# Optimization experiments

Hardware: AMD Instinct MI355X
Metric: run time of the kernel (lower is better)

## Reference

```python
import jax, jax.numpy as jnp
import numpy as np

N = 8192
EPS = 1e-12

def setup_inputs() -> dict:
    key = jax.random.key(0)
    k1, k2 = jax.random.split(key)
    var_1 = jax.random.normal(k1, (N,), dtype=jnp.float32)          # e.g. bb mass
    var_2 = jax.random.uniform(k2, (N,), dtype=jnp.float32)          # classifier output in (0,1)
    normedweight = jnp.ones((N,), dtype=jnp.float32)                 # weights sum to N
    return {"var_1": var_1, "var_2": var_2, "normedweight": normedweight, "power": 2}


def reference(var_1, var_2, normedweight, power):
    # Pairwise absolute difference matrices [N, N]
    amat = jnp.abs(var_1[:, None] - var_1[None, :])
    bmat = jnp.abs(var_2[:, None] - var_2[None, :])

    # Weighted row means (weight broadcasts along columns, mean over axis=1)
    amatavg = jnp.mean(amat * normedweight, axis=1)                  # [N]
    bmatavg = jnp.mean(bmat * normedweight, axis=1)                  # [N]

    # Double centering: minuend_1[i,j] = avg[j], minuend_2[i,j] = avg[i]
    Amat = amat - amatavg[None, :] - amatavg[:, None] + jnp.mean(amatavg * normedweight)
    Bmat = bmat - bmatavg[None, :] - bmatavg[:, None] + jnp.mean(bmatavg * normedweight)

    ABavg = jnp.abs(jnp.mean(Amat * Bmat * normedweight, axis=1))    # [N]
    AAavg = jnp.mean(Amat * Amat * normedweight, axis=1)             # [N]
    BBavg = jnp.mean(Bmat * Bmat * normedweight, axis=1)             # [N]

    num = jnp.mean(ABavg * normedweight)
    den = jnp.abs(jnp.mean(AAavg * normedweight) * jnp.mean(BBavg * normedweight))

    if power == 1:
        dCorr = num / jnp.sqrt(den + EPS)
    elif power == 2:
        dCorr = num ** 2 / (den + EPS)
    else:
        dCorr = (num / jnp.sqrt(jnp.mean(AAavg * normedweight) * jnp.mean(BBavg * normedweight)) + EPS) ** power

    # Original clamps NaN and negative results to 0
    dCorr = jnp.where(jnp.isnan(dCorr), jnp.float32(0.0), dCorr)
    dCorr = jnp.maximum(dCorr, jnp.float32(0.0))
    return dCorr
```

## Files before the change

### kernel.cpp

```cpp
#include <hip/hip_runtime.h>
#include <math.h>


#define NN 8192
#define BLK 256
#define RPT 4
#define ROWS_PER_BLOCK 16
#define GRIDX 512
#define CSPLIT 4
#define SEGC 2048
#define ITERS 8
#define NBLK (GRIDX * CSPLIT)
#define MIDB 32
#define RPT2 8
#define G2BLK (NN / RPT2)
#define INV_N (1.0f / NN)
#define NSC 9

__device__ __forceinline__ void p1_elem(
    float aj, float bj, float wj,
    const float* __restrict__ ai, const float* __restrict__ bi,
    float* __restrict__ sa, float* __restrict__ sb) {
#pragma unroll
  for (int m = 0; m < RPT; ++m) {
    sa[m] = fmaf(fabsf(ai[m] - aj), wj, sa[m]);
    sb[m] = fmaf(fabsf(bi[m] - bj), wj, sb[m]);
  }
}

__global__ __launch_bounds__(BLK) void k_pass1(
    const float* __restrict__ a, const float* __restrict__ b,
    const float* __restrict__ w,
    float* __restrict__ pa, float* __restrict__ pb,
    double* __restrict__ gpa, double* __restrict__ gpb) {
  const int lane = threadIdx.x & 63;
  const int wv = threadIdx.x >> 6;
  const int i0 = blockIdx.x * ROWS_PER_BLOCK + wv * RPT;
  const int seg = blockIdx.y;

  float ai[RPT], bi[RPT], sa[RPT], sb[RPT];
#pragma unroll
  for (int m = 0; m < RPT; ++m) {
    ai[m] = a[i0 + m]; bi[m] = b[i0 + m];
    sa[m] = 0.f; sb[m] = 0.f;
  }

  const int jb = seg * SEGC;
  const float4* a4 = (const float4*)(a + jb) + lane;
  const float4* b4 = (const float4*)(b + jb) + lane;
  const float4* w4 = (const float4*)(w + jb) + lane;

  float4 A0 = a4[0], B0 = b4[0], W0 = w4[0];
#pragma unroll 1
  for (int k = 0; k < ITERS - 1; ++k) {
    const int nx = (k + 1) * 64;
    const float4 A1 = a4[nx], B1 = b4[nx], W1 = w4[nx];
    p1_elem(A0.x, B0.x, W0.x, ai, bi, sa, sb);
    p1_elem(A0.y, B0.y, W0.y, ai, bi, sa, sb);
    p1_elem(A0.z, B0.z, W0.z, ai, bi, sa, sb);
    p1_elem(A0.w, B0.w, W0.w, ai, bi, sa, sb);
    A0 = A1; B0 = B1; W0 = W1;
  }
  p1_elem(A0.x, B0.x, W0.x, ai, bi, sa, sb);
  p1_elem(A0.y, B0.y, W0.y, ai, bi, sa, sb);
  p1_elem(A0.z, B0.z, W0.z, ai, bi, sa, sb);
  p1_elem(A0.w, B0.w, W0.w, ai, bi, sa, sb);

#pragma unroll
  for (int off = 32; off >= 1; off >>= 1) {
#pragma unroll
    for (int m = 0; m < RPT; ++m) {
      sa[m] += __shfl_xor(sa[m], off);
      sb[m] += __shfl_xor(sb[m], off);
    }
  }

  __shared__ double gla[4], glb[4];
  if (lane == 0) {
#pragma unroll
    for (int m = 0; m < RPT; ++m) {
      pa[seg * NN + i0 + m] = sa[m];
      pb[seg * NN + i0 + m] = sb[m];
    }
    double da = 0.0, db = 0.0;
#pragma unroll
    for (int m = 0; m < RPT; ++m) {
      const double wi = (double)w[i0 + m];
      da += (double)sa[m] * wi;
      db += (double)sb[m] * wi;
    }
    gla[wv] = da; glb[wv] = db;
  }
  __syncthreads();
  if (threadIdx.x == 0) {
    const int bid = blockIdx.y * GRIDX + blockIdx.x;
    gpa[bid] = gla[0] + gla[1] + gla[2] + gla[3];
    gpb[bid] = glb[0] + glb[1] + glb[2] + glb[3];
  }
}

__global__ __launch_bounds__(BLK) void k_mid(
    const float* __restrict__ a, const float* __restrict__ b,
    const float* __restrict__ w,
    const float* __restrict__ pa, const float* __restrict__ pb,
    const double* __restrict__ gpa, const double* __restrict__ gpb,
    float* __restrict__ rr, float* __restrict__ ss, float* __restrict__ wrv,
    double* __restrict__ scal, double* __restrict__ hs) {
  const int lane = threadIdx.x & 63;
  const int wv = threadIdx.x >> 6;

  __shared__ double gsum[2];
  if (wv < 2) {
    const double* g = wv ? gpb : gpa;
    double s = 0.0;
    for (int k = 0; k < NBLK / 64; ++k) s += g[lane + 64 * k];
#pragma unroll
    for (int off = 32; off >= 1; off >>= 1) s += __shfl_xor(s, off);
    if (lane == 0) gsum[wv] = s;
  }
  __syncthreads();
  const double n2 = (double)NN * (double)NN;
  const float ha = (float)(0.5 * gsum[0] / n2);
  const float hb = (float)(0.5 * gsum[1] / n2);
  if (blockIdx.x == 0 && threadIdx.x == 0) { hs[0] = (double)ha; hs[1] = (double)hb; }

  const int i = blockIdx.x * BLK + threadIdx.x;
  const float av = (pa[i] + pa[NN + i] + pa[2 * NN + i] + pa[3 * NN + i]) * INV_N;
  const float bv = (pb[i] + pb[NN + i] + pb[2 * NN + i] + pb[3 * NN + i]) * INV_N;
  const float ri = av - ha;
  const float si = bv - hb;
  const float wi = w[i], aiv = a[i], biv = b[i];
  rr[i] = ri;  ss[i] = si;  wrv[i] = wi * ri;

  double p[NSC];
  p[0] = (double)wi;
  p[1] = (double)wi * aiv;
  p[2] = (double)wi * aiv * aiv;
  p[3] = (double)wi * biv;
  p[4] = (double)wi * biv * biv;
  p[5] = (double)wi * ri;
  p[6] = (double)wi * si;
  p[7] = (double)wi * ri * ri;
  p[8] = (double)wi * si * si;
#pragma unroll
  for (int off = 32; off >= 1; off >>= 1) {
#pragma unroll
    for (int t = 0; t < NSC; ++t) p[t] += __shfl_xor(p[t], off);
  }
  __shared__ double lp[NSC][4];
  if (lane == 0) {
#pragma unroll
    for (int t = 0; t < NSC; ++t) lp[t][wv] = p[t];
  }
  __syncthreads();
  if (threadIdx.x == 0) {
#pragma unroll
    for (int t = 0; t < NSC; ++t)
      scal[t * MIDB + blockIdx.x] = lp[t][0] + lp[t][1] + lp[t][2] + lp[t][3];
  }
}

__global__ __launch_bounds__(BLK) void k_pass2(
    const float* __restrict__ a, const float* __restrict__ b,
    const float* __restrict__ w,
    const float* __restrict__ rr, const float* __restrict__ ss,
    const float* __restrict__ wrv,
    const double* __restrict__ scal, const double* __restrict__ hs,
    double* __restrict__ fAB) {
  const int lane = threadIdx.x & 63;
  const int wv = threadIdx.x >> 6;
  const int i0 = blockIdx.x * RPT2;

  double Wd   = scal[0 * MIDB + (lane & 31)];
  double Swrd = scal[5 * MIDB + (lane & 31)];
  double Swsd = scal[6 * MIDB + (lane & 31)];
#pragma unroll
  for (int off = 16; off >= 1; off >>= 1) {
    Wd   += __shfl_xor(Wd, off);
    Swrd += __shfl_xor(Swrd, off);
    Swsd += __shfl_xor(Swsd, off);
  }

  float ai[RPT2], bi[RPT2], q[RPT2];
#pragma unroll
  for (int m = 0; m < RPT2; ++m) {
    ai[m] = a[i0 + m]; bi[m] = b[i0 + m];
    q[m] = 0.f;
  }

  const int jb = wv * SEGC;
  const float4* a4 = (const float4*)(a + jb)   + lane;
  const float4* b4 = (const float4*)(b + jb)   + lane;
  const float4* w4 = (const float4*)(w + jb)   + lane;
  const float4* r4 = (const float4*)(wrv + jb) + lane;
  const float4* s4 = (const float4*)(ss + jb)  + lane;

#pragma unroll 1
  for (int k = 0; k < ITERS; ++k) {
    const int ix = k * 64;
    const float4 A = a4[ix], B = b4[ix], Wt = w4[ix], R = r4[ix], S = s4[ix];
#define P2E(e)                                                  \
    {                                                           \
      _Pragma("unroll")                                         \
      for (int m = 0; m < RPT2; ++m) {                          \
        const float ta = ai[m] - A.e;                           \
        const float tb = bi[m] - B.e;                           \
        const float wdp = fmaf(Wt.e, fabsf(ta), -R.e);          \
        const float ep = fabsf(tb) - S.e;                       \
        q[m] = fmaf(wdp, ep, q[m]);                             \
      }                                                         \
    }
    P2E(x) P2E(y) P2E(z) P2E(w)
#undef P2E
  }

#pragma unroll
  for (int off = 32; off >= 1; off >>= 1) {
#pragma unroll
    for (int m = 0; m < RPT2; ++m) q[m] += __shfl_xor(q[m], off);
  }

  __shared__ float lq[CSPLIT][RPT2];
  __shared__ double lab[RPT2];
  if (lane == 0) {
#pragma unroll
    for (int m = 0; m < RPT2; ++m) lq[wv][m] = q[m];
  }
  __syncthreads();
  if (threadIdx.x < RPT2) {
    const int m = threadIdx.x;
    const double Qi = (double)lq[0][m] + lq[1][m] + lq[2][m] + lq[3][m];
    const double ha = hs[0], hb = hs[1];
    const double ri = (double)rr[i0 + m];
    const double si = (double)ss[i0 + m];
    const double wi = (double)w[i0 + m];
    const double P0a = (ri + ha) * (double)NN;
    const double P0b = (si + hb) * (double)NN;
    const double TAB = Qi - si * (P0a - Swrd) - ri * (P0b - Swsd) + ri * si * Wd;
    lab[m] = fabs(TAB) * wi;
  }
  __syncthreads();
  if (threadIdx.x == 0) {
    double s = 0.0;
#pragma unroll
    for (int m = 0; m < RPT2; ++m) s += lab[m];
    fAB[blockIdx.x] = s;
  }
}

__global__ __launch_bounds__(BLK) void k_fin(
    const double* __restrict__ fAB, const double* __restrict__ scal,
    const double* __restrict__ hs, const int* __restrict__ powerPtr,
    float* __restrict__ out) {
  const int lane = threadIdx.x & 63;
  const int wv = threadIdx.x >> 6;

  double ab = 0.0;
#pragma unroll
  for (int k = 0; k < G2BLK / BLK; ++k) ab += fAB[threadIdx.x + k * BLK];
#pragma unroll
  for (int off = 32; off >= 1; off >>= 1) ab += __shfl_xor(ab, off);
  __shared__ double l[4];
  __shared__ double sc[NSC];
  if (lane == 0) l[wv] = ab;
  if (threadIdx.x < NSC) {
    double s = 0.0;
    for (int k = 0; k < MIDB; ++k) s += scal[threadIdx.x * MIDB + k];
    sc[threadIdx.x] = s;
  }
  __syncthreads();

  if (threadIdx.x == 0) {
    const double n2 = (double)NN * (double)NN;
    const double sab = l[0] + l[1] + l[2] + l[3];
    const double W = sc[0], Ma1 = sc[1], Ma2 = sc[2], Mb1 = sc[3], Mb2 = sc[4];
    const double Swr = sc[5], Sws = sc[6], Swr2 = sc[7], Sws2 = sc[8];
    const double ha = hs[0], hb = hs[1];

    const double S_AA = 2.0 * W * Ma2 - 2.0 * Ma1 * Ma1
                      - 4.0 * (double)NN * (Swr2 + ha * Swr)
                      + 2.0 * W * Swr2 + 2.0 * Swr * Swr;
    const double S_BB = 2.0 * W * Mb2 - 2.0 * Mb1 * Mb1
                      - 4.0 * (double)NN * (Sws2 + hb * Sws)
                      + 2.0 * W * Sws2 + 2.0 * Sws * Sws;

    const double num = sab / n2;
    const double mAA = S_AA / n2;
    const double mBB = S_BB / n2;
    const double den = fabs(mAA * mBB);
    const int p = powerPtr[0];
    double d;
    if (p == 1) {
      d = num / sqrt(den + 1e-12);
    } else if (p == 2) {
      d = (num * num) / (den + 1e-12);
    } else {
      d = pow(num / sqrt(mAA * mBB) + 1e-12, (double)p);
    }
    if (isnan(d)) d = 0.0;
    if (d < 0.0) d = 0.0;
    out[0] = (float)d;
  }
}

extern "C" void kernel_launch(void* const* d_in, const int* in_sizes, int n_in,
                              void* d_out, int out_size, void* d_ws, size_t ws_size,
                              hipStream_t stream) {
  const float* a = (const float*)d_in[0];
  const float* b = (const float*)d_in[1];
  const float* w = (const float*)d_in[2];
  const int* power = (const int*)d_in[3];
  float* out = (float*)d_out;

  double* dws = (double*)d_ws;
  double* gpa  = dws;
  double* gpb  = gpa + NBLK;
  double* scal = gpb + NBLK;
  double* hs   = scal + NSC * MIDB;
  double* fAB  = hs + 2;
  float* fp    = (float*)(fAB + G2BLK);
  float* pa    = fp;
  float* pb    = pa + 4 * NN;
  float* rr    = pb + 4 * NN;
  float* ss    = rr + NN;
  float* wrv   = ss + NN;

  const dim3 grid(GRIDX, CSPLIT);
  k_pass1<<<grid, BLK, 0, stream>>>(a, b, w, pa, pb, gpa, gpb);
  k_mid<<<MIDB, BLK, 0, stream>>>(a, b, w, pa, pb, gpa, gpb, rr, ss, wrv, scal, hs);
  k_pass2<<<G2BLK, BLK, 0, stream>>>(a, b, w, rr, ss, wrv, scal, hs, fAB);
  k_fin<<<1, BLK, 0, stream>>>(fAB, scal, hs, power, out);
}
```

Baseline: 36.42 us.

## Fuse row-mean reduction and moments into pass1, eliminating mid kernel

Pass1 now computes full row sums within a block, with four waves each covering a quarter of the columns and eight rows per block. It writes the row averages and per-block moment partials directly, so the separate middle kernel and its launch go away. Pass2 re-reduces the per-block moments itself to get the grand mean and centering sums, and applies the centering on the fly in its inner loop. This trades one kernel launch and an extra round trip through global memory for redundant moment reductions in every pass2 block and a few extra flops per column.

After: 36.25 us. No clear change (-0.4%).

```diff
diff --git a/kernel.cpp b/kernel.cpp
--- a/kernel.cpp
+++ b/kernel.cpp
@@ -4,209 +4,163 @@
 
 #define NN 8192
 #define BLK 256
-#define RPT 4
-#define ROWS_PER_BLOCK 16
-#define GRIDX 512
-#define CSPLIT 4
-#define SEGC 2048
-#define ITERS 8
-#define NBLK (GRIDX * CSPLIT)
-#define MIDB 32
-#define RPT2 8
-#define G2BLK (NN / RPT2)
-#define INV_N (1.0f / NN)
+#define NW 4
+#define RP 8
+#define GBLK (NN / RP)
+#define SEGC (NN / NW)
+#define ITERS (SEGC / 256)
 #define NSC 9
-
-__device__ __forceinline__ void p1_elem(
-    float aj, float bj, float wj,
-    const float* __restrict__ ai, const float* __restrict__ bi,
-    float* __restrict__ sa, float* __restrict__ sb) {
-#pragma unroll
-  for (int m = 0; m < RPT; ++m) {
-    sa[m] = fmaf(fabsf(ai[m] - aj), wj, sa[m]);
-    sb[m] = fmaf(fabsf(bi[m] - bj), wj, sb[m]);
-  }
-}
 
 __global__ __launch_bounds__(BLK) void k_pass1(
     const float* __restrict__ a, const float* __restrict__ b,
     const float* __restrict__ w,
-    float* __restrict__ pa, float* __restrict__ pb,
-    double* __restrict__ gpa, double* __restrict__ gpb) {
+    float* __restrict__ avga, float* __restrict__ avgb,
+    double* __restrict__ gmom) {
   const int lane = threadIdx.x & 63;
   const int wv = threadIdx.x >> 6;
-  const int i0 = blockIdx.x * ROWS_PER_BLOCK + wv * RPT;
-  const int seg = blockIdx.y;
-
-  float ai[RPT], bi[RPT], sa[RPT], sb[RPT];
-#pragma unroll
-  for (int m = 0; m < RPT; ++m) {
+  const int i0 = blockIdx.x * RP;
+
+  float ai[RP], bi[RP], sa[RP], sb[RP];
+#pragma unroll
+  for (int m = 0; m < RP; ++m) {
     ai[m] = a[i0 + m]; bi[m] = b[i0 + m];
     sa[m] = 0.f; sb[m] = 0.f;
   }
 
-  const int jb = seg * SEGC;
+  const int jb = wv * SEGC;
   const float4* a4 = (const float4*)(a + jb) + lane;
   const float4* b4 = (const float4*)(b + jb) + lane;
   const float4* w4 = (const float4*)(w + jb) + lane;
 
-  float4 A0 = a4[0], B0 = b4[0], W0 = w4[0];
 #pragma unroll 1
-  for (int k = 0; k < ITERS - 1; ++k) {
-    const int nx = (k + 1) * 64;
-    const float4 A1 = a4[nx], B1 = b4[nx], W1 = w4[nx];
-    p1_elem(A0.x, B0.x, W0.x, ai, bi, sa, sb);
-    p1_elem(A0.y, B0.y, W0.y, ai, bi, sa, sb);
-    p1_elem(A0.z, B0.z, W0.z, ai, bi, sa, sb);
-    p1_elem(A0.w, B0.w, W0.w, ai, bi, sa, sb);
-    A0 = A1; B0 = B1; W0 = W1;
-  }
-  p1_elem(A0.x, B0.x, W0.x, ai, bi, sa, sb);
-  p1_elem(A0.y, B0.y, W0.y, ai, bi, sa, sb);
-  p1_elem(A0.z, B0.z, W0.z, ai, bi, sa, sb);
-  p1_elem(A0.w, B0.w, W0.w, ai, bi, sa, sb);
-
-#pragma unroll
-  for (int off = 32; off >= 1; off >>= 1) {
-#pragma unroll
-    for (int m = 0; m < RPT; ++m) {
+  for (int k = 0; k < ITERS; ++k) {
+    const int ix = k * 64;
+    const float4 A = a4[ix], B = b4[ix], Wt = w4[ix];
+#define P1E(e)                                              \
+    {                                                       \
+      _Pragma("unroll")                                     \
+      for (int m = 0; m < RP; ++m) {                        \
+        sa[m] = fmaf(fabsf(ai[m] - A.e), Wt.e, sa[m]);      \
+        sb[m] = fmaf(fabsf(bi[m] - B.e), Wt.e, sb[m]);      \
+      }                                                     \
+    }
+    P1E(x) P1E(y) P1E(z) P1E(w)
+#undef P1E
+  }
+
+#pragma unroll
+  for (int off = 32; off >= 1; off >>= 1) {
+#pragma unroll
+    for (int m = 0; m < RP; ++m) {
       sa[m] += __shfl_xor(sa[m], off);
       sb[m] += __shfl_xor(sb[m], off);
     }
   }
 
-  __shared__ double gla[4], glb[4];
+  __shared__ float lsa[NW][RP], lsb[NW][RP];
+  __shared__ double dmom[RP][NSC];
   if (lane == 0) {
 #pragma unroll
-    for (int m = 0; m < RPT; ++m) {
-      pa[seg * NN + i0 + m] = sa[m];
-      pb[seg * NN + i0 + m] = sb[m];
-    }
-    double da = 0.0, db = 0.0;
-#pragma unroll
-    for (int m = 0; m < RPT; ++m) {
-      const double wi = (double)w[i0 + m];
-      da += (double)sa[m] * wi;
-      db += (double)sb[m] * wi;
-    }
-    gla[wv] = da; glb[wv] = db;
+    for (int m = 0; m < RP; ++m) { lsa[wv][m] = sa[m]; lsb[wv][m] = sb[m]; }
+  }
+  __syncthreads();
+  if (threadIdx.x < RP) {
+    const int m = threadIdx.x;
+    const double rowA = (double)lsa[0][m] + lsa[1][m] + lsa[2][m] + lsa[3][m];
+    const double rowB = (double)lsb[0][m] + lsb[1][m] + lsb[2][m] + lsb[3][m];
+    const double avA = rowA * (1.0 / NN);
+    const double avB = rowB * (1.0 / NN);
+    avga[i0 + m] = (float)avA;
+    avgb[i0 + m] = (float)avB;
+    const double wi = (double)w[i0 + m];
+    const double aiv = (double)a[i0 + m];
+    const double biv = (double)b[i0 + m];
+    dmom[m][0] = wi;
+    dmom[m][1] = wi * aiv;
+    dmom[m][2] = wi * aiv * aiv;
+    dmom[m][3] = wi * biv;
+    dmom[m][4] = wi * biv * biv;
+    dmom[m][5] = wi * avA;
+    dmom[m][6] = wi * avA * avA;
+    dmom[m][7] = wi * avB;
+    dmom[m][8] = wi * avB * avB;
   }
   __syncthreads();
   if (threadIdx.x == 0) {
-    const int bid = blockIdx.y * GRIDX + blockIdx.x;
-    gpa[bid] = gla[0] + gla[1] + gla[2] + gla[3];
-    gpb[bid] = glb[0] + glb[1] + glb[2] + glb[3];
-  }
-}
-
-__global__ __launch_bounds__(BLK) void k_mid(
-    const float* __restrict__ a, const float* __restrict__ b,
-    const float* __restrict__ w,
-    const float* __restrict__ pa, const float* __restrict__ pb,
-    const double* __restrict__ gpa, const double* __restrict__ gpb,
-    float* __restrict__ rr, float* __restrict__ ss, float* __restrict__ wrv,
-    double* __restrict__ scal, double* __restrict__ hs) {
-  const int lane = threadIdx.x & 63;
-  const int wv = threadIdx.x >> 6;
-
-  __shared__ double gsum[2];
-  if (wv < 2) {
-    const double* g = wv ? gpb : gpa;
-    double s = 0.0;
-    for (int k = 0; k < NBLK / 64; ++k) s += g[lane + 64 * k];
-#pragma unroll
-    for (int off = 32; off >= 1; off >>= 1) s += __shfl_xor(s, off);
-    if (lane == 0) gsum[wv] = s;
-  }
-  __syncthreads();
-  const double n2 = (double)NN * (double)NN;
-  const float ha = (float)(0.5 * gsum[0] / n2);
-  const float hb = (float)(0.5 * gsum[1] / n2);
-  if (blockIdx.x == 0 && threadIdx.x == 0) { hs[0] = (double)ha; hs[1] = (double)hb; }
-
-  const int i = blockIdx.x * BLK + threadIdx.x;
-  const float av = (pa[i] + pa[NN + i] + pa[2 * NN + i] + pa[3 * NN + i]) * INV_N;
-  const float bv = (pb[i] + pb[NN + i] + pb[2 * NN + i] + pb[3 * NN + i]) * INV_N;
-  const float ri = av - ha;
-  const float si = bv - hb;
-  const float wi = w[i], aiv = a[i], biv = b[i];
-  rr[i] = ri;  ss[i] = si;  wrv[i] = wi * ri;
-
-  double p[NSC];
-  p[0] = (double)wi;
-  p[1] = (double)wi * aiv;
-  p[2] = (double)wi * aiv * aiv;
-  p[3] = (double)wi * biv;
-  p[4] = (double)wi * biv * biv;
-  p[5] = (double)wi * ri;
-  p[6] = (double)wi * si;
-  p[7] = (double)wi * ri * ri;
-  p[8] = (double)wi * si * si;
-#pragma unroll
-  for (int off = 32; off >= 1; off >>= 1) {
-#pragma unroll
-    for (int t = 0; t < NSC; ++t) p[t] += __shfl_xor(p[t], off);
-  }
-  __shared__ double lp[NSC][4];
-  if (lane == 0) {
-#pragma unroll
-    for (int t = 0; t < NSC; ++t) lp[t][wv] = p[t];
-  }
-  __syncthreads();
-  if (threadIdx.x == 0) {
-#pragma unroll
-    for (int t = 0; t < NSC; ++t)
-      scal[t * MIDB + blockIdx.x] = lp[t][0] + lp[t][1] + lp[t][2] + lp[t][3];
+#pragma unroll
+    for (int t = 0; t < NSC; ++t) {
+      double s = 0.0;
+#pragma unroll
+      for (int m = 0; m < RP; ++m) s += dmom[m][t];
+      gmom[t * GBLK + blockIdx.x] = s;
+    }
   }
 }
 
 __global__ __launch_bounds__(BLK) void k_pass2(
     const float* __restrict__ a, const float* __restrict__ b,
     const float* __restrict__ w,
-    const float* __restrict__ rr, const float* __restrict__ ss,
-    const float* __restrict__ wrv,
-    const double* __restrict__ scal, const double* __restrict__ hs,
+    const float* __restrict__ avga, const float* __restrict__ avgb,
+    const double* __restrict__ gmom,
     double* __restrict__ fAB) {
   const int lane = threadIdx.x & 63;
   const int wv = threadIdx.x >> 6;
-  const int i0 = blockIdx.x * RPT2;
-
-  double Wd   = scal[0 * MIDB + (lane & 31)];
-  double Swrd = scal[5 * MIDB + (lane & 31)];
-  double Swsd = scal[6 * MIDB + (lane & 31)];
-#pragma unroll
-  for (int off = 16; off >= 1; off >>= 1) {
-    Wd   += __shfl_xor(Wd, off);
-    Swrd += __shfl_xor(Swrd, off);
-    Swsd += __shfl_xor(Swsd, off);
-  }
-
-  float ai[RPT2], bi[RPT2], q[RPT2];
-#pragma unroll
-  for (int m = 0; m < RPT2; ++m) {
+  const int i0 = blockIdx.x * RP;
+
+  double pW = 0.0, pU = 0.0, pV = 0.0;
+#pragma unroll
+  for (int k = 0; k < GBLK / BLK; ++k) {
+    const int t = threadIdx.x + k * BLK;
+    pW += gmom[0 * GBLK + t];
+    pU += gmom[5 * GBLK + t];
+    pV += gmom[7 * GBLK + t];
+  }
+#pragma unroll
+  for (int off = 32; off >= 1; off >>= 1) {
+    pW += __shfl_xor(pW, off);
+    pU += __shfl_xor(pU, off);
+    pV += __shfl_xor(pV, off);
+  }
+  __shared__ double l3[3][NW];
+  if (lane == 0) { l3[0][wv] = pW; l3[1][wv] = pU; l3[2][wv] = pV; }
+  __syncthreads();
+  const double Wd   = l3[0][0] + l3[0][1] + l3[0][2] + l3[0][3];
+  const double Sua1 = l3[1][0] + l3[1][1] + l3[1][2] + l3[1][3];
+  const double Sub1 = l3[2][0] + l3[2][1] + l3[2][2] + l3[2][3];
+  const double had = Sua1 / (2.0 * NN);
+  const double hbd = Sub1 / (2.0 * NN);
+  const double Swrd = Sua1 - had * Wd;
+  const double Swsd = Sub1 - hbd * Wd;
+  const float ha = (float)had, hb = (float)hbd;
+
+  float ai[RP], bi[RP], q[RP];
+#pragma unroll
+  for (int m = 0; m < RP; ++m) {
     ai[m] = a[i0 + m]; bi[m] = b[i0 + m];
     q[m] = 0.f;
   }
 
   const int jb = wv * SEGC;
-  const float4* a4 = (const float4*)(a + jb)   + lane;
-  const float4* b4 = (const float4*)(b + jb)   + lane;
-  const float4* w4 = (const float4*)(w + jb)   + lane;
-  const float4* r4 = (const float4*)(wrv + jb) + lane;
-  const float4* s4 = (const float4*)(ss + jb)  + lane;
+  const float4* a4 = (const float4*)(a + jb)    + lane;
+  const float4* b4 = (const float4*)(b + jb)    + lane;
+  const float4* w4 = (const float4*)(w + jb)    + lane;
+  const float4* c4 = (const float4*)(avga + jb) + lane;
+  const float4* d4 = (const float4*)(avgb + jb) + lane;
 
 #pragma unroll 1
   for (int k = 0; k < ITERS; ++k) {
     const int ix = k * 64;
-    const float4 A = a4[ix], B = b4[ix], Wt = w4[ix], R = r4[ix], S = s4[ix];
+    const float4 A = a4[ix], B = b4[ix], Wt = w4[ix], CA = c4[ix], CB = d4[ix];
 #define P2E(e)                                                  \
     {                                                           \
+      const float wrj = Wt.e * (CA.e - ha);                     \
+      const float sj  = CB.e - hb;                              \
       _Pragma("unroll")                                         \
-      for (int m = 0; m < RPT2; ++m) {                          \
+      for (int m = 0; m < RP; ++m) {                            \
         const float ta = ai[m] - A.e;                           \
         const float tb = bi[m] - B.e;                           \
-        const float wdp = fmaf(Wt.e, fabsf(ta), -R.e);          \
-        const float ep = fabsf(tb) - S.e;                       \
+        const float wdp = fmaf(Wt.e, fabsf(ta), -wrj);          \
+        const float ep = fabsf(tb) - sj;                        \
         q[m] = fmaf(wdp, ep, q[m]);                             \
       }                                                         \
     }
@@ -217,25 +171,26 @@
 #pragma unroll
   for (int off = 32; off >= 1; off >>= 1) {
 #pragma unroll
-    for (int m = 0; m < RPT2; ++m) q[m] += __shfl_xor(q[m], off);
-  }
-
-  __shared__ float lq[CSPLIT][RPT2];
-  __shared__ double lab[RPT2];
+    for (int m = 0; m < RP; ++m) q[m] += __shfl_xor(q[m], off);
+  }
+
+  __shared__ float lq[NW][RP];
+  __shared__ double lab[RP];
   if (lane == 0) {
 #pragma unroll
-    for (int m = 0; m < RPT2; ++m) lq[wv][m] = q[m];
-  }
-  __syncthreads();
-  if (threadIdx.x < RPT2) {
+    for (int m = 0; m < RP; ++m) lq[wv][m] = q[m];
+  }
+  __syncthreads();
+  if (threadIdx.x < RP) {
     const int m = threadIdx.x;
     const double Qi = (double)lq[0][m] + lq[1][m] + lq[2][m] + lq[3][m];
-    const double ha = hs[0], hb = hs[1];
-    const double ri = (double)rr[i0 + m];
-    const double si = (double)ss[i0 + m];
+    const double avA = (double)avga[i0 + m];
+    const double avB = (double)avgb[i0 + m];
+    const double ri = avA - had;
+    const double si = avB - hbd;
     const double wi = (double)w[i0 + m];
-    const double P0a = (ri + ha) * (double)NN;
-    const double P0b = (si + hb) * (double)NN;
+    const double P0a = avA * (double)NN;
+    const double P0b = avB * (double)NN;
     const double TAB = Qi - si * (P0a - Swrd) - ri * (P0b - Swsd) + ri * si * Wd;
     lab[m] = fabs(TAB) * wi;
   }
@@ -243,39 +198,57 @@
   if (threadIdx.x == 0) {
     double s = 0.0;
 #pragma unroll
-    for (int m = 0; m < RPT2; ++m) s += lab[m];
+    for (int m = 0; m < RP; ++m) s += lab[m];
     fAB[blockIdx.x] = s;
   }
 }
 
 __global__ __launch_bounds__(BLK) void k_fin(
-    const double* __restrict__ fAB, const double* __restrict__ scal,
-    const double* __restrict__ hs, const int* __restrict__ powerPtr,
-    float* __restrict__ out) {
+    const double* __restrict__ fAB, const double* __restrict__ gmom,
+    const int* __restrict__ powerPtr, float* __restrict__ out) {
   const int lane = threadIdx.x & 63;
   const int wv = threadIdx.x >> 6;
 
   double ab = 0.0;
 #pragma unroll
-  for (int k = 0; k < G2BLK / BLK; ++k) ab += fAB[threadIdx.x + k * BLK];
-#pragma unroll
-  for (int off = 32; off >= 1; off >>= 1) ab += __shfl_xor(ab, off);
-  __shared__ double l[4];
-  __shared__ double sc[NSC];
-  if (lane == 0) l[wv] = ab;
-  if (threadIdx.x < NSC) {
+  for (int k = 0; k < GBLK / BLK; ++k) ab += fAB[threadIdx.x + k * BLK];
+  double p[NSC];
+#pragma unroll
+  for (int t = 0; t < NSC; ++t) {
     double s = 0.0;
-    for (int k = 0; k < MIDB; ++k) s += scal[threadIdx.x * MIDB + k];
-    sc[threadIdx.x] = s;
+#pragma unroll
+    for (int k = 0; k < GBLK / BLK; ++k) s += gmom[t * GBLK + threadIdx.x + k * BLK];
+    p[t] = s;
+  }
+#pragma unroll
+  for (int off = 32; off >= 1; off >>= 1) {
+    ab += __shfl_xor(ab, off);
+#pragma unroll
+    for (int t = 0; t < NSC; ++t) p[t] += __shfl_xor(p[t], off);
+  }
+  __shared__ double l[NW];
+  __shared__ double lp[NSC][NW];
+  if (lane == 0) {
+    l[wv] = ab;
+#pragma unroll
+    for (int t = 0; t < NSC; ++t) lp[t][wv] = p[t];
   }
   __syncthreads();
 
   if (threadIdx.x == 0) {
     const double n2 = (double)NN * (double)NN;
     const double sab = l[0] + l[1] + l[2] + l[3];
+    double sc[NSC];
+#pragma unroll
+    for (int t = 0; t < NSC; ++t) sc[t] = lp[t][0] + lp[t][1] + lp[t][2] + lp[t][3];
     const double W = sc[0], Ma1 = sc[1], Ma2 = sc[2], Mb1 = sc[3], Mb2 = sc[4];
-    const double Swr = sc[5], Sws = sc[6], Swr2 = sc[7], Sws2 = sc[8];
-    const double ha = hs[0], hb = hs[1];
+    const double Sua1 = sc[5], Sua2 = sc[6], Sub1 = sc[7], Sub2 = sc[8];
+    const double ha = Sua1 / (2.0 * NN);
+    const double hb = Sub1 / (2.0 * NN);
+    const double Swr  = Sua1 - ha * W;
+    const double Sws  = Sub1 - hb * W;
+    const double Swr2 = Sua2 - 2.0 * ha * Sua1 + ha * ha * W;
+    const double Sws2 = Sub2 - 2.0 * hb * Sub1 + hb * hb * W;
 
     const double S_AA = 2.0 * W * Ma2 - 2.0 * Ma1 * Ma1
                       - 4.0 * (double)NN * (Swr2 + ha * Swr)
@@ -288,14 +261,14 @@
     const double mAA = S_AA / n2;
     const double mBB = S_BB / n2;
     const double den = fabs(mAA * mBB);
-    const int p = powerPtr[0];
+    const int pw = powerPtr[0];
     double d;
-    if (p == 1) {
+    if (pw == 1) {
       d = num / sqrt(den + 1e-12);
-    } else if (p == 2) {
+    } else if (pw == 2) {
       d = (num * num) / (den + 1e-12);
     } else {
-      d = pow(num / sqrt(mAA * mBB) + 1e-12, (double)p);
+      d = pow(num / sqrt(mAA * mBB) + 1e-12, (double)pw);
     }
     if (isnan(d)) d = 0.0;
     if (d < 0.0) d = 0.0;
@@ -313,21 +286,13 @@
   float* out = (float*)d_out;
 
   double* dws = (double*)d_ws;
-  double* gpa  = dws;
-  double* gpb  = gpa + NBLK;
-  double* scal = gpb + NBLK;
-  double* hs   = scal + NSC * MIDB;
-  double* fAB  = hs + 2;
-  float* fp    = (float*)(fAB + G2BLK);
-  float* pa    = fp;
-  float* pb    = pa + 4 * NN;
-  float* rr    = pb + 4 * NN;
-  float* ss    = rr + NN;
-  float* wrv   = ss + NN;
-
-  const dim3 grid(GRIDX, CSPLIT);
-  k_pass1<<<grid, BLK, 0, stream>>>(a, b, w, pa, pb, gpa, gpb);
-  k_mid<<<MIDB, BLK, 0, stream>>>(a, b, w, pa, pb, gpa, gpb, rr, ss, wrv, scal, hs);
-  k_pass2<<<G2BLK, BLK, 0, stream>>>(a, b, w, rr, ss, wrv, scal, hs, fAB);
-  k_fin<<<1, BLK, 0, stream>>>(fAB, scal, hs, power, out);
-}
+  double* gmom = dws;
+  double* fAB  = gmom + NSC * GBLK;
+  float* fp    = (float*)(fAB + GBLK);
+  float* avga  = fp;
+  float* avgb  = avga + NN;
+
+  k_pass1<<<GBLK, BLK, 0, stream>>>(a, b, w, avga, avgb, gmom);
+  k_pass2<<<GBLK, BLK, 0, stream>>>(a, b, w, avga, avgb, gmom, fAB);
+  k_fin<<<1, BLK, 0, stream>>>(fAB, gmom, power, out);
+}
```
